# Kernel tuning notes

Hardware: AMD Instinct MI355X
Metric: run time of the kernel (lower is better)

## Reference

```python
import jax, jax.numpy as jnp
import numpy as np

B, T, D, U = 32, 2048, 512, 512


def setup_inputs() -> dict:
    key = jax.random.key(0)
    ks = jax.random.split(key, 6)
    value = jax.random.normal(ks[0], (B, T, D), dtype=jnp.float32)
    query = jax.random.normal(ks[1], (B, D), dtype=jnp.float32)
    mask = jax.random.randint(ks[2], (B, T), 0, 2, dtype=jnp.int32)
    # Glorot-ish scaled dense weights (no bias, matching Dense(use_bias=False))
    W1 = jax.random.normal(ks[3], (D, U), dtype=jnp.float32) * (1.0 / np.sqrt(D))
    W2 = jax.random.normal(ks[4], (D, U), dtype=jnp.float32) * (1.0 / np.sqrt(D))
    V = jax.random.normal(ks[5], (U,), dtype=jnp.float32) * (1.0 / np.sqrt(U))
    return {"value": value, "query": query, "mask": mask, "W1": W1, "W2": W2, "V": V}


def reference(value, query, mask, W1, W2, V):
    # Additive (Bahdanau) attention scores: u[b,t] = V . tanh(value[b,t] @ W1 + query[b] @ W2)
    w1_key = jnp.einsum('btd,du->btu', value, W1)          # [B, T, U]
    w2_query = jnp.einsum('bd,du->bu', query, W2)          # [B, U]
    u = jnp.einsum('btu,u->bt', jnp.tanh(w1_key + w2_query[:, None, :]), V)  # [B, T]
    # Masking: add -1e20 where mask == 0 (same as keras reference)
    u = u + (1.0 - mask.astype(u.dtype)) * jnp.asarray(-1e20, dtype=u.dtype)
    a = jax.nn.softmax(u, axis=1)                          # [B, T]
    # Pointer extraction: gather value row at argmax of attention weights
    idx = jnp.argmax(a, axis=1)                            # [B]
    context = jnp.take_along_axis(value, idx[:, None, None], axis=1)[:, 0, :]  # [B, D]
    return (context, a)
```

## Files before the change

kernel.cpp:

```cpp
#include <hip/hip_runtime.h>
#include <hip/hip_fp16.h>
#include <stdint.h>

#define B_ 32
#define T_ 2048
#define D_ 512
#define U_ 512
#define M_ (B_ * T_)
#define MAXC 4

#define BK 32
#define SAW 40

typedef _Float16 half8   __attribute__((ext_vector_type(8)));
typedef _Float16 half4_t __attribute__((ext_vector_type(4)));
typedef float   floatx4  __attribute__((ext_vector_type(4)));

__device__ __forceinline__ float tanh_fast(float x) {
    float ax = fabsf(x);
    float e  = __expf(2.0f * ax);
    float t  = 1.0f - 2.0f / (e + 1.0f);
    return copysignf(t, x);
}

__device__ __forceinline__ void gld_lds16(const void* gsrc, void* lds_dst) {
    typedef __attribute__((address_space(1))) const char gch;
    typedef __attribute__((address_space(3))) char lch;
    __builtin_amdgcn_global_load_lds((const gch*)(uintptr_t)gsrc,
                                     (lch*)(uint32_t)(uintptr_t)lds_dst,
                                     16, 0, 0);
}

__global__ __launch_bounds__(256)
void k_prep(const float* __restrict__ W1, const float* __restrict__ query,
            const float* __restrict__ W2, _Float16* __restrict__ W1T,
            float* __restrict__ w2q) {
    const int bid = blockIdx.x;
    const int tid = threadIdx.x;
    if (bid < 64) {
        __shared__ float tile[64][65];
        const int bx = bid & 7;
        const int by = bid >> 3;
        const int k0 = bx * 64, n0 = by * 64;
        const int tx = tid & 63;
        const int ty = tid >> 6;
#pragma unroll
        for (int i = 0; i < 16; ++i) {
            int r = ty * 16 + i;
            tile[r][tx] = W1[(size_t)(k0 + r) * U_ + n0 + tx];
        }
        __syncthreads();
#pragma unroll
        for (int i = 0; i < 16; ++i) {
            int r = ty * 16 + i;
            W1T[(size_t)(n0 + r) * D_ + k0 + tx] = (_Float16)tile[tx][r];
        }
    } else {
        __shared__ float sq[D_];
        __shared__ float part[128];
        const int id = bid - 64;
        const int b  = id >> 2;
        const int nq = id & 3;
        sq[tid]       = query[b * D_ + tid];
        sq[tid + 256] = query[b * D_ + tid + 256];
        __syncthreads();
        const int n  = nq * 128 + (tid & 127);
        const int dh = tid >> 7;
        float acc = 0.f;
        const int d0 = dh * 256;
#pragma unroll 16
        for (int d = d0; d < d0 + 256; ++d)
            acc = fmaf(sq[d], W2[(size_t)d * U_ + n], acc);
        if (dh == 1) part[tid & 127] = acc;
        __syncthreads();
        if (dh == 0) w2q[b * U_ + n] = acc + part[tid];
    }
}

__global__ __launch_bounds__(512, 5)
void k_gemm_u(const float* __restrict__ value,
              const _Float16* __restrict__ W1T,
              const float* __restrict__ w2q,
              const float* __restrict__ Vv,
              float* __restrict__ u_part) {
    __shared__ __align__(16) _Float16 sA[64 * SAW];
    __shared__ __align__(16) _Float16 sB[256 * BK];
    __shared__ float sRed[8][64];

    const int tid  = threadIdx.x;
    const int wave = tid >> 6;
    const int lane = tid & 63;
    const int l15  = lane & 15;
    const int lg   = lane >> 4;
    const int bx   = blockIdx.x;
    const int sl   = (bx >> 3) & 1;
    const int rg   = ((bx >> 4) << 3) | (bx & 7);
    const int m0   = rg * 64;
    const int b    = m0 >> 11;

    const int bnl  = l15;
    const int bhi8 = lg * 8;

    const int ar = tid >> 3;
    const int ac = (tid & 7) * 4;
    const float* aptr = value + (size_t)(m0 + ar) * D_ + ac;

    floatx4 acc[4][2];
    const floatx4 zero4 = {0.f, 0.f, 0.f, 0.f};
#pragma unroll
    for (int i = 0; i < 4; ++i)
#pragma unroll
        for (int j = 0; j < 2; ++j) acc[i][j] = zero4;

    for (int it = 0; it < 16; ++it) {
        const int k0 = it * BK;
        __syncthreads();
        {
            const floatx4 v4 = *(const floatx4*)(aptr + k0);
            half4_t h;
            h[0] = (_Float16)v4[0]; h[1] = (_Float16)v4[1];
            h[2] = (_Float16)v4[2]; h[3] = (_Float16)v4[3];
            *(half4_t*)(&sA[ar * SAW + ac]) = h;
        }
#pragma unroll
        for (int jj = 0; jj < 2; ++jj) {
            const int inst = wave * 2 + jj;
            const int n = sl * 256 + inst * 16 + bnl;
            gld_lds16(W1T + (size_t)n * D_ + k0 + bhi8, (void*)(&sB[inst * 512]));
        }
        __syncthreads();

        half8 af[4], bf[2];
#pragma unroll
        for (int mi = 0; mi < 4; ++mi)
            af[mi] = *(const half8*)(&sA[(mi * 16 + l15) * SAW + lg * 8]);
#pragma unroll
        for (int ni = 0; ni < 2; ++ni) {
            const int inst = wave * 2 + ni;
            bf[ni] = *(const half8*)(&sB[inst * 512 + (lg * 16 + l15) * 8]);
        }
#pragma unroll
        for (int ni = 0; ni < 2; ++ni)
#pragma unroll
            for (int mi = 0; mi < 4; ++mi)
                acc[mi][ni] = __builtin_amdgcn_mfma_f32_16x16x32_f16(
                    af[mi], bf[ni], acc[mi][ni], 0, 0, 0);
    }

    float ps[4][4];
#pragma unroll
    for (int mi = 0; mi < 4; ++mi)
#pragma unroll
        for (int j = 0; j < 4; ++j) ps[mi][j] = 0.f;

#pragma unroll
    for (int ni = 0; ni < 2; ++ni) {
        const int n = sl * 256 + wave * 32 + ni * 16 + l15;
        const float w2 = w2q[b * U_ + n];
        const float vv = Vv[n];
#pragma unroll
        for (int mi = 0; mi < 4; ++mi)
#pragma unroll
            for (int j = 0; j < 4; ++j)
                ps[mi][j] += vv * tanh_fast(acc[mi][ni][j] + w2);
    }
#pragma unroll
    for (int off = 1; off < 16; off <<= 1)
#pragma unroll
        for (int mi = 0; mi < 4; ++mi)
#pragma unroll
            for (int j = 0; j < 4; ++j)
                ps[mi][j] += __shfl_xor(ps[mi][j], off, 64);

    if (l15 == 0) {
#pragma unroll
        for (int mi = 0; mi < 4; ++mi)
#pragma unroll
            for (int j = 0; j < 4; ++j)
                sRed[wave][mi * 16 + lg * 4 + j] = ps[mi][j];
    }
    __syncthreads();
    if (tid < 64) {
        float s = 0.f;
#pragma unroll
        for (int w = 0; w < 8; ++w) s += sRed[w][tid];
        u_part[(size_t)sl * M_ + m0 + tid] = s;
    }
}

__global__ __launch_bounds__(256)
void k_post(const float* __restrict__ u_part, const int* __restrict__ mask,
            const float* __restrict__ value, const float* __restrict__ W1,
            const float* __restrict__ w2q, const float* __restrict__ Vv,
            float* __restrict__ a_out, float* __restrict__ ctx_out) {
    __shared__ float sx[T_];
    __shared__ float rv[4];
    __shared__ int   ri[4];
    __shared__ float s_scalar;
    __shared__ int   s_cand[MAXC];
    __shared__ float s_score[MAXC];
    __shared__ __align__(16) float vrows[MAXC][D_];
    __shared__ int   s_t;

    const int b = blockIdx.x;
    const int tid = threadIdx.x;
    const int wave = tid >> 6, lane = tid & 63;

#pragma unroll
    for (int i = 0; i < 8; ++i) {
        const int t = tid * 8 + i;
        float x = u_part[b * T_ + t] + u_part[M_ + b * T_ + t];
        if (mask[b * T_ + t] == 0) x = -1e20f;
        sx[t] = x;
    }
    __syncthreads();

    for (int r = 0; r < MAXC; ++r) {
        float v = -INFINITY; int vi = 0;
#pragma unroll
        for (int i = 0; i < 8; ++i) {
            const int t = tid * 8 + i;
            const float x = sx[t];
            if (x > v) { v = x; vi = t; }
        }
        for (int off = 32; off > 0; off >>= 1) {
            const float ov = __shfl_down(v, off, 64);
            const int   oi = __shfl_down(vi, off, 64);
            if (ov > v || (ov == v && oi < vi)) { v = ov; vi = oi; }
        }
        if (lane == 0) { rv[wave] = v; ri[wave] = vi; }
        __syncthreads();
        if (tid == 0) {
            float bv = rv[0]; int bi = ri[0];
            for (int w = 1; w < 4; ++w)
                if (rv[w] > bv || (rv[w] == bv && ri[w] < bi)) { bv = rv[w]; bi = ri[w]; }
            s_cand[r] = bi;
            if (r == 0) s_scalar = bv;
            sx[bi] = -INFINITY;
        }
        __syncthreads();
    }
    const float mx = s_scalar;

    float zloc = 0.f;
    float evals[8];
#pragma unroll
    for (int i = 0; i < 8; ++i) {
        const int t = tid * 8 + i;
        float x = u_part[b * T_ + t] + u_part[M_ + b * T_ + t];
        if (mask[b * T_ + t] == 0) x = -1e20f;
        const float e = __expf(x - mx);
        evals[i] = e;
        zloc += e;
    }
    for (int off = 32; off > 0; off >>= 1) zloc += __shfl_down(zloc, off, 64);
    if (lane == 0) rv[wave] = zloc;
    __syncthreads();
    if (tid == 0) s_scalar = 1.0f / (rv[0] + rv[1] + rv[2] + rv[3]);
    __syncthreads();
    const float rz = s_scalar;
#pragma unroll
    for (int i = 0; i < 8; ++i) {
        const int t = tid * 8 + i;
        a_out[b * T_ + t] = evals[i] * rz;
    }

#pragma unroll
    for (int ci = 0; ci < MAXC; ++ci) {
        const int t = s_cand[ci];
        vrows[ci][tid]       = value[((size_t)b * T_ + t) * D_ + tid];
        vrows[ci][tid + 256] = value[((size_t)b * T_ + t) * D_ + tid + 256];
    }
    __syncthreads();

    float dots[2][MAXC];
#pragma unroll
    for (int j = 0; j < 2; ++j)
#pragma unroll
        for (int ci = 0; ci < MAXC; ++ci) dots[j][ci] = 0.f;

    for (int d4 = 0; d4 < D_; d4 += 4) {
        floatx4 vr[MAXC];
#pragma unroll
        for (int ci = 0; ci < MAXC; ++ci)
            vr[ci] = *(const floatx4*)(&vrows[ci][d4]);
#pragma unroll
        for (int k = 0; k < 4; ++k) {
            const float w0 = W1[(size_t)(d4 + k) * U_ + tid];
            const float w1 = W1[(size_t)(d4 + k) * U_ + tid + 256];
#pragma unroll
            for (int ci = 0; ci < MAXC; ++ci) {
                dots[0][ci] = fmaf(vr[ci][k], w0, dots[0][ci]);
                dots[1][ci] = fmaf(vr[ci][k], w1, dots[1][ci]);
            }
        }
    }
    float sc[MAXC];
#pragma unroll
    for (int ci = 0; ci < MAXC; ++ci) {
        const float n0v = Vv[tid]       * tanhf(dots[0][ci] + w2q[b * U_ + tid]);
        const float n1v = Vv[tid + 256] * tanhf(dots[1][ci] + w2q[b * U_ + tid + 256]);
        sc[ci] = n0v + n1v;
    }
#pragma unroll
    for (int ci = 0; ci < MAXC; ++ci)
        for (int off = 32; off > 0; off >>= 1)
            sc[ci] += __shfl_down(sc[ci], off, 64);
    __syncthreads();
    if (lane == 0) {
#pragma unroll
        for (int ci = 0; ci < MAXC; ++ci)
            vrows[ci][wave] = sc[ci];
    }
    __syncthreads();
    if (tid == 0) {
#pragma unroll
        for (int ci = 0; ci < MAXC; ++ci) {
            const int t = s_cand[ci];
            float s = vrows[ci][0] + vrows[ci][1] + vrows[ci][2] + vrows[ci][3];
            if (mask[b * T_ + t] == 0) s = -1e20f;
            s_score[ci] = s;
        }
        float bv = s_score[0]; int bt = s_cand[0];
        for (int i = 1; i < MAXC; ++i) {
            if (s_score[i] > bv || (s_score[i] == bv && s_cand[i] < bt)) {
                bv = s_score[i]; bt = s_cand[i];
            }
        }
        s_t = bt;
    }
    __syncthreads();

    const int t = s_t;
    ctx_out[b * D_ + tid]       = value[((size_t)b * T_ + t) * D_ + tid];
    ctx_out[b * D_ + tid + 256] = value[((size_t)b * T_ + t) * D_ + tid + 256];
}

extern "C" void kernel_launch(void* const* d_in, const int* in_sizes, int n_in,
                              void* d_out, int out_size, void* d_ws, size_t ws_size,
                              hipStream_t stream) {
    const float* value = (const float*)d_in[0];
    const float* query = (const float*)d_in[1];
    const int*   mask  = (const int*)d_in[2];
    const float* W1    = (const float*)d_in[3];
    const float* W2    = (const float*)d_in[4];
    const float* Vv    = (const float*)d_in[5];

    char* ws = (char*)d_ws;
    _Float16* W1T    = (_Float16*)ws;
    float*    w2q    = (float*)(ws + 524288);
    float*    u_part = (float*)(ws + 524288 + 65536);

    float* ctx_out = (float*)d_out;
    float* a_out   = (float*)d_out + B_ * D_;

    hipLaunchKernelGGL(k_prep,   dim3(192), dim3(256), 0, stream,
                       W1, query, W2, W1T, w2q);
    hipLaunchKernelGGL(k_gemm_u, dim3(2048), dim3(512), 0, stream,
                       value, W1T, w2q, Vv, u_part);
    hipLaunchKernelGGL(k_post,   dim3(32), dim3(256), 0, stream,
                       u_part, mask, value, W1, w2q, Vv, a_out, ctx_out);
}
```

Before: 331.7 us.

## Widen GEMM tile to full U with double-buffered async loads; split post-processing

The score GEMM now gives each 1024-thread block 128 rows and all 512 output columns. Before, the U dimension was split across two blocks, so every row of value was read twice; now it is read once. A and B tiles are loaded with async global-to-LDS copies into swizzled, double-buffered shared memory, and A is converted to fp16 when fragments are read. The candidate re-scoring moves out of the single-block-per-batch post kernel into a 256-block kernel that accumulates with atomics, followed by a small final selection kernel. The trade-offs are much higher LDS use per block, which limits residency, and two extra kernel launches.

```diff
diff --git a/kernel.cpp b/kernel.cpp
--- a/kernel.cpp
+++ b/kernel.cpp
@@ -8,12 +8,9 @@
 #define U_ 512
 #define M_ (B_ * T_)
 #define MAXC 4
-
 #define BK 32
-#define SAW 40
 
 typedef _Float16 half8   __attribute__((ext_vector_type(8)));
-typedef _Float16 half4_t __attribute__((ext_vector_type(4)));
 typedef float   floatx4  __attribute__((ext_vector_type(4)));
 
 __device__ __forceinline__ float tanh_fast(float x) {
@@ -39,11 +36,9 @@
     const int tid = threadIdx.x;
     if (bid < 64) {
         __shared__ float tile[64][65];
-        const int bx = bid & 7;
-        const int by = bid >> 3;
+        const int bx = bid & 7, by = bid >> 3;
         const int k0 = bx * 64, n0 = by * 64;
-        const int tx = tid & 63;
-        const int ty = tid >> 6;
+        const int tx = tid & 63, ty = tid >> 6;
 #pragma unroll
         for (int i = 0; i < 16; ++i) {
             int r = ty * 16 + i;
@@ -77,85 +72,101 @@
     }
 }
 
-__global__ __launch_bounds__(512, 5)
+__global__ __launch_bounds__(1024, 4)
 void k_gemm_u(const float* __restrict__ value,
               const _Float16* __restrict__ W1T,
               const float* __restrict__ w2q,
               const float* __restrict__ Vv,
-              float* __restrict__ u_part) {
-    __shared__ __align__(16) _Float16 sA[64 * SAW];
-    __shared__ __align__(16) _Float16 sB[256 * BK];
-    __shared__ float sRed[8][64];
+              float* __restrict__ u_out) {
+    __shared__ __align__(16) float    sA[2][128 * 32];
+    __shared__ __align__(16) _Float16 sB[2][512 * 32];
+    __shared__ float sRed[16][64];
 
     const int tid  = threadIdx.x;
-    const int wave = tid >> 6;
-    const int lane = tid & 63;
-    const int l15  = lane & 15;
-    const int lg   = lane >> 4;
-    const int bx   = blockIdx.x;
-    const int sl   = (bx >> 3) & 1;
-    const int rg   = ((bx >> 4) << 3) | (bx & 7);
-    const int m0   = rg * 64;
+    const int wv   = tid >> 6;
+    const int l    = tid & 63;
+    const int l15  = l & 15;
+    const int lg   = l >> 4;
+    const int m0   = blockIdx.x * 128;
     const int b    = m0 >> 11;
-
-    const int bnl  = l15;
-    const int bhi8 = lg * 8;
-
-    const int ar = tid >> 3;
-    const int ac = (tid & 7) * 4;
-    const float* aptr = value + (size_t)(m0 + ar) * D_ + ac;
-
-    floatx4 acc[4][2];
+    const int wr   = (wv >> 3) * 64;
+    const int wc   = (wv & 7) * 64;
+
+    const int a_row = tid >> 3;
+    const int a_lu  = (l & 7) ^ (l >> 3);
+    const float* a_src = value + (size_t)(m0 + a_row) * D_ + a_lu * 4;
+    const int b_lu = (l & 3) ^ ((l >> 3) & 3);
+    const int b_n0 = (l >> 2);
+
+#define ISSUE(c, buf)                                                          \
+    {                                                                          \
+        gld_lds16(a_src + (c) * BK, (void*)(&sA[buf][wv * 256]));              \
+        _Pragma("unroll")                                                      \
+        for (int j = 0; j < 2; ++j) {                                          \
+            const int inst = wv * 2 + j;                                       \
+            const int n = inst * 16 + b_n0;                                    \
+            gld_lds16(W1T + (size_t)n * D_ + (c) * BK + b_lu * 8,              \
+                      (void*)(&sB[buf][inst * 512]));                          \
+        }                                                                      \
+    }
+
+    ISSUE(0, 0);
+
+    floatx4 acc[4][4];
     const floatx4 zero4 = {0.f, 0.f, 0.f, 0.f};
 #pragma unroll
     for (int i = 0; i < 4; ++i)
 #pragma unroll
-        for (int j = 0; j < 2; ++j) acc[i][j] = zero4;
-
-    for (int it = 0; it < 16; ++it) {
-        const int k0 = it * BK;
-        __syncthreads();
-        {
-            const floatx4 v4 = *(const floatx4*)(aptr + k0);
-            half4_t h;
-            h[0] = (_Float16)v4[0]; h[1] = (_Float16)v4[1];
-            h[2] = (_Float16)v4[2]; h[3] = (_Float16)v4[3];
-            *(half4_t*)(&sA[ar * SAW + ac]) = h;
-        }
-#pragma unroll
-        for (int jj = 0; jj < 2; ++jj) {
-            const int inst = wave * 2 + jj;
-            const int n = sl * 256 + inst * 16 + bnl;
-            gld_lds16(W1T + (size_t)n * D_ + k0 + bhi8, (void*)(&sB[inst * 512]));
-        }
-        __syncthreads();
-
-        half8 af[4], bf[2];
-#pragma unroll
-        for (int mi = 0; mi < 4; ++mi)
-            af[mi] = *(const half8*)(&sA[(mi * 16 + l15) * SAW + lg * 8]);
-#pragma unroll
-        for (int ni = 0; ni < 2; ++ni) {
-            const int inst = wave * 2 + ni;
-            bf[ni] = *(const half8*)(&sB[inst * 512 + (lg * 16 + l15) * 8]);
-        }
-#pragma unroll
-        for (int ni = 0; ni < 2; ++ni)
+        for (int j = 0; j < 4; ++j) acc[i][j] = zero4;
+
+    __syncthreads();
+
+    for (int c = 0; c < 16; ++c) {
+        const int cur = c & 1;
+        if (c < 15) ISSUE(c + 1, cur ^ 1);
+
+        half8 af[4];
+#pragma unroll
+        for (int mi = 0; mi < 4; ++mi) {
+            const int row = wr + mi * 16 + l15;
+            const int r7  = l15 & 7;
+            const int p0  = (lg * 2) ^ r7;
+            const int p1  = (lg * 2 + 1) ^ r7;
+            const floatx4 x0 = *(const floatx4*)(&sA[cur][row * 32 + p0 * 4]);
+            const floatx4 x1 = *(const floatx4*)(&sA[cur][row * 32 + p1 * 4]);
+            half8 h;
+#pragma unroll
+            for (int q = 0; q < 4; ++q) {
+                h[q]     = (_Float16)x0[q];
+                h[4 + q] = (_Float16)x1[q];
+            }
+            af[mi] = h;
+        }
+        half8 bf[4];
+#pragma unroll
+        for (int ni = 0; ni < 4; ++ni) {
+            const int n = wc + ni * 16 + l15;
+            const int p = lg ^ ((l15 >> 1) & 3);
+            bf[ni] = *(const half8*)(&sB[cur][n * 32 + p * 8]);
+        }
+#pragma unroll
+        for (int ni = 0; ni < 4; ++ni)
 #pragma unroll
             for (int mi = 0; mi < 4; ++mi)
                 acc[mi][ni] = __builtin_amdgcn_mfma_f32_16x16x32_f16(
                     af[mi], bf[ni], acc[mi][ni], 0, 0, 0);
-    }
+        __syncthreads();
+    }
+#undef ISSUE
 
     float ps[4][4];
 #pragma unroll
     for (int mi = 0; mi < 4; ++mi)
 #pragma unroll
         for (int j = 0; j < 4; ++j) ps[mi][j] = 0.f;
-
-#pragma unroll
-    for (int ni = 0; ni < 2; ++ni) {
-        const int n = sl * 256 + wave * 32 + ni * 16 + l15;
+#pragma unroll
+    for (int ni = 0; ni < 4; ++ni) {
+        const int n = wc + ni * 16 + l15;
         const float w2 = w2q[b * U_ + n];
         const float vv = Vv[n];
 #pragma unroll
@@ -177,39 +188,37 @@
         for (int mi = 0; mi < 4; ++mi)
 #pragma unroll
             for (int j = 0; j < 4; ++j)
-                sRed[wave][mi * 16 + lg * 4 + j] = ps[mi][j];
-    }
-    __syncthreads();
-    if (tid < 64) {
+                sRed[wv][mi * 16 + lg * 4 + j] = ps[mi][j];
+    }
+    __syncthreads();
+    if (tid < 128) {
+        const int half = tid >> 6, lr = tid & 63;
         float s = 0.f;
 #pragma unroll
-        for (int w = 0; w < 8; ++w) s += sRed[w][tid];
-        u_part[(size_t)sl * M_ + m0 + tid] = s;
+        for (int cw = 0; cw < 8; ++cw) s += sRed[half * 8 + cw][lr];
+        u_out[m0 + tid] = s;
     }
 }
 
 __global__ __launch_bounds__(256)
-void k_post(const float* __restrict__ u_part, const int* __restrict__ mask,
-            const float* __restrict__ value, const float* __restrict__ W1,
-            const float* __restrict__ w2q, const float* __restrict__ Vv,
-            float* __restrict__ a_out, float* __restrict__ ctx_out) {
+void k_post(const float* __restrict__ u, const int* __restrict__ mask,
+            float* __restrict__ a_out, int* __restrict__ cand_t,
+            float* __restrict__ cand_score) {
     __shared__ float sx[T_];
     __shared__ float rv[4];
     __shared__ int   ri[4];
     __shared__ float s_scalar;
-    __shared__ int   s_cand[MAXC];
-    __shared__ float s_score[MAXC];
-    __shared__ __align__(16) float vrows[MAXC][D_];
-    __shared__ int   s_t;
 
     const int b = blockIdx.x;
     const int tid = threadIdx.x;
     const int wave = tid >> 6, lane = tid & 63;
 
+    if (tid < MAXC) cand_score[b * MAXC + tid] = 0.f;
+
 #pragma unroll
     for (int i = 0; i < 8; ++i) {
         const int t = tid * 8 + i;
-        float x = u_part[b * T_ + t] + u_part[M_ + b * T_ + t];
+        float x = u[b * T_ + t];
         if (mask[b * T_ + t] == 0) x = -1e20f;
         sx[t] = x;
     }
@@ -234,7 +243,7 @@
             float bv = rv[0]; int bi = ri[0];
             for (int w = 1; w < 4; ++w)
                 if (rv[w] > bv || (rv[w] == bv && ri[w] < bi)) { bv = rv[w]; bi = ri[w]; }
-            s_cand[r] = bi;
+            cand_t[b * MAXC + r] = bi;
             if (r == 0) s_scalar = bv;
             sx[bi] = -INFINITY;
         }
@@ -247,7 +256,7 @@
 #pragma unroll
     for (int i = 0; i < 8; ++i) {
         const int t = tid * 8 + i;
-        float x = u_part[b * T_ + t] + u_part[M_ + b * T_ + t];
+        float x = u[b * T_ + t];
         if (mask[b * T_ + t] == 0) x = -1e20f;
         const float e = __expf(x - mx);
         evals[i] = e;
@@ -264,73 +273,83 @@
         const int t = tid * 8 + i;
         a_out[b * T_ + t] = evals[i] * rz;
     }
+}
+
+__global__ __launch_bounds__(256)
+void k_resc(const float* __restrict__ value, const float* __restrict__ W1,
+            const float* __restrict__ w2q, const float* __restrict__ Vv,
+            const int* __restrict__ cand_t, float* __restrict__ cand_score) {
+    __shared__ __align__(16) float vrows[MAXC][D_];
+    __shared__ float part[4][MAXC][64];
+    const int b  = blockIdx.x >> 3;
+    const int nc = blockIdx.x & 7;
+    const int tid = threadIdx.x;
 
 #pragma unroll
     for (int ci = 0; ci < MAXC; ++ci) {
-        const int t = s_cand[ci];
+        const int t = cand_t[b * MAXC + ci];
         vrows[ci][tid]       = value[((size_t)b * T_ + t) * D_ + tid];
         vrows[ci][tid + 256] = value[((size_t)b * T_ + t) * D_ + tid + 256];
     }
     __syncthreads();
 
-    float dots[2][MAXC];
-#pragma unroll
-    for (int j = 0; j < 2; ++j)
-#pragma unroll
-        for (int ci = 0; ci < MAXC; ++ci) dots[j][ci] = 0.f;
-
-    for (int d4 = 0; d4 < D_; d4 += 4) {
-        floatx4 vr[MAXC];
+    const int q  = tid >> 6;
+    const int nl = tid & 63;
+    const int n  = nc * 64 + nl;
+    float dq[MAXC] = {0.f, 0.f, 0.f, 0.f};
+    const int d0 = q * 128;
+#pragma unroll 8
+    for (int d = d0; d < d0 + 128; ++d) {
+        const float w = W1[(size_t)d * U_ + n];
 #pragma unroll
         for (int ci = 0; ci < MAXC; ++ci)
-            vr[ci] = *(const floatx4*)(&vrows[ci][d4]);
-#pragma unroll
-        for (int k = 0; k < 4; ++k) {
-            const float w0 = W1[(size_t)(d4 + k) * U_ + tid];
-            const float w1 = W1[(size_t)(d4 + k) * U_ + tid + 256];
-#pragma unroll
-            for (int ci = 0; ci < MAXC; ++ci) {
-                dots[0][ci] = fmaf(vr[ci][k], w0, dots[0][ci]);
-                dots[1][ci] = fmaf(vr[ci][k], w1, dots[1][ci]);
-            }
-        }
-    }
-    float sc[MAXC];
-#pragma unroll
-    for (int ci = 0; ci < MAXC; ++ci) {
-        const float n0v = Vv[tid]       * tanhf(dots[0][ci] + w2q[b * U_ + tid]);
-        const float n1v = Vv[tid + 256] * tanhf(dots[1][ci] + w2q[b * U_ + tid + 256]);
-        sc[ci] = n0v + n1v;
-    }
-#pragma unroll
-    for (int ci = 0; ci < MAXC; ++ci)
-        for (int off = 32; off > 0; off >>= 1)
-            sc[ci] += __shfl_down(sc[ci], off, 64);
-    __syncthreads();
-    if (lane == 0) {
-#pragma unroll
-        for (int ci = 0; ci < MAXC; ++ci)
-            vrows[ci][wave] = sc[ci];
-    }
-    __syncthreads();
+            dq[ci] = fmaf(vrows[ci][d], w, dq[ci]);
+    }
+#pragma unroll
+    for (int ci = 0; ci < MAXC; ++ci) part[q][ci][nl] = dq[ci];
+    __syncthreads();
+
+    if (q == 0) {
+        const float w2 = w2q[b * U_ + n];
+        const float vv = Vv[n];
+        float sc[MAXC];
+#pragma unroll
+        for (int ci = 0; ci < MAXC; ++ci) {
+            const float dot = part[0][ci][nl] + part[1][ci][nl]
+                            + part[2][ci][nl] + part[3][ci][nl];
+            sc[ci] = vv * tanhf(dot + w2);
+        }
+#pragma unroll
+        for (int off = 1; off < 64; off <<= 1)
+#pragma unroll
+            for (int ci = 0; ci < MAXC; ++ci)
+                sc[ci] += __shfl_xor(sc[ci], off, 64);
+        if (nl == 0) {
+#pragma unroll
+            for (int ci = 0; ci < MAXC; ++ci)
+                atomicAdd(&cand_score[b * MAXC + ci], sc[ci]);
+        }
+    }
+}
+
+__global__ __launch_bounds__(256)
+void k_fin(const float* __restrict__ value, const int* __restrict__ mask,
+           const int* __restrict__ cand_t, const float* __restrict__ cand_score,
+           float* __restrict__ ctx_out) {
+    __shared__ int s_t;
+    const int b = blockIdx.x;
+    const int tid = threadIdx.x;
     if (tid == 0) {
-#pragma unroll
-        for (int ci = 0; ci < MAXC; ++ci) {
-            const int t = s_cand[ci];
-            float s = vrows[ci][0] + vrows[ci][1] + vrows[ci][2] + vrows[ci][3];
+        float bv = -INFINITY; int bt = cand_t[b * MAXC];
+        for (int i = 0; i < MAXC; ++i) {
+            const int   t = cand_t[b * MAXC + i];
+            float s = cand_score[b * MAXC + i];
             if (mask[b * T_ + t] == 0) s = -1e20f;
-            s_score[ci] = s;
-        }
-        float bv = s_score[0]; int bt = s_cand[0];
-        for (int i = 1; i < MAXC; ++i) {
-            if (s_score[i] > bv || (s_score[i] == bv && s_cand[i] < bt)) {
-                bv = s_score[i]; bt = s_cand[i];
-            }
+            if (s > bv || (s == bv && t < bt)) { bv = s; bt = t; }
         }
         s_t = bt;
     }
     __syncthreads();
-
     const int t = s_t;
     ctx_out[b * D_ + tid]       = value[((size_t)b * T_ + t) * D_ + tid];
     ctx_out[b * D_ + tid + 256] = value[((size_t)b * T_ + t) * D_ + tid + 256];
@@ -347,17 +366,23 @@
     const float* Vv    = (const float*)d_in[5];
 
     char* ws = (char*)d_ws;
-    _Float16* W1T    = (_Float16*)ws;
-    float*    w2q    = (float*)(ws + 524288);
-    float*    u_part = (float*)(ws + 524288 + 65536);
+    _Float16* W1T        = (_Float16*)ws;
+    float*    w2q        = (float*)(ws + 524288);
+    float*    u_ws       = (float*)(ws + 589824);
+    int*      cand_t     = (int*)(ws + 851968);
+    float*    cand_score = (float*)(ws + 852480);
 
     float* ctx_out = (float*)d_out;
     float* a_out   = (float*)d_out + B_ * D_;
 
     hipLaunchKernelGGL(k_prep,   dim3(192), dim3(256), 0, stream,
                        W1, query, W2, W1T, w2q);
-    hipLaunchKernelGGL(k_gemm_u, dim3(2048), dim3(512), 0, stream,
-                       value, W1T, w2q, Vv, u_part);
+    hipLaunchKernelGGL(k_gemm_u, dim3(M_ / 128), dim3(1024), 0, stream,
+                       value, W1T, w2q, Vv, u_ws);
     hipLaunchKernelGGL(k_post,   dim3(32), dim3(256), 0, stream,
-                       u_part, mask, value, W1, w2q, Vv, a_out, ctx_out);
-}
+                       u_ws, mask, a_out, cand_t, cand_score);
+    hipLaunchKernelGGL(k_resc,   dim3(256), dim3(256), 0, stream,
+                       value, W1, w2q, Vv, cand_t, cand_score);
+    hipLaunchKernelGGL(k_fin,    dim3(32), dim3(256), 0, stream,
+                       value, mask, cand_t, cand_score, ctx_out);
+}
```

After: 270.0 us. 1.23x faster.
